# Kernel tuning notes

Measured on AMD Instinct MI355X. Metric: run time of the kernel, lower is better.

## Reference

```python
import jax, jax.numpy as jnp
import numpy as np

# ---- fixed constants from stft2hcfp.__init__ ----
FS = 16000.0; FR = 2.0; FC = 27.5; TC = 1.0 / 4487.0; NPO = 48
N = int(FS / FR)                      # 8000 FFT length
HALF_N = int(round(N / 2))            # 4000
SQRT_N = float(np.sqrt(N))
HIGH_FREQ_IDX = int(round(1.0 / TC / FR) + 1)   # 2245
HIGH_QUEF_IDX = int(round(FS / FC)) + 1         # 583
CUT_Q = int(round(FS * TC))           # 4  (cepstrum cutoff)
TOTAL_BINS = 4 * 88                   # 352 log-freq bins
NUM_HARMONIC = 5

def _central_freqs():
    stop = 1.0 / TC
    nest = int(np.ceil(np.log2(stop / FC)) * NPO)
    cf = []
    for i in range(nest):
        c = FC * 2.0 ** (float(i) / NPO)
        if c < stop:
            cf.append(c)
        else:
            break
    return cf

CF = _central_freqs()   # 353 central frequencies
NEST = len(CF)

def _freq_matrix():
    # triangular log-frequency filterbank over linear freq axis
    f = (FS * np.linspace(0, 0.5, HALF_N, endpoint=True))[:HIGH_FREQ_IDX]
    W = np.zeros((NEST - 1, len(f)), np.float32)
    for i in range(1, NEST - 1):
        l = int(round(CF[i - 1] / FR)); r = int(round(CF[i + 1] / FR) + 1)
        if l >= r - 1:
            W[i, l] = 1.0
        else:
            for j in range(l, r):
                if CF[i - 1] < f[j] < CF[i]:
                    W[i, j] = (f[j] - CF[i - 1]) / (CF[i] - CF[i - 1])
                elif CF[i] < f[j] < CF[i + 1]:
                    W[i, j] = (CF[i + 1] - f[j]) / (CF[i + 1] - CF[i])
    return W

def _quef_matrix():
    q = np.arange(HIGH_QUEF_IDX) / FS + 1e-6
    fq = 1.0 / q
    W = np.zeros((NEST - 1, len(fq)), np.float32)
    for i in range(1, NEST - 1):
        for j in range(int(round(FS / CF[i + 1])), int(round(FS / CF[i - 1]) + 1)):
            if j >= len(fq):
                continue
            if CF[i - 1] < fq[j] < CF[i]:
                W[i, j] = (fq[j] - CF[i - 1]) / (CF[i] - CF[i - 1])
            elif CF[i] < fq[j] < CF[i + 1]:
                W[i, j] = (CF[i + 1] - fq[j]) / (CF[i + 1] - CF[i])
    return W

# harmonic shift indices: closest central freq to (k+1)*27.5 Hz, k=0..5
HIDS = [int(np.argmin(np.abs(np.asarray(CF) - (k + 1) * FC))) for k in range(NUM_HARMONIC + 1)]


def _nonlinear(x, g, cutoff):
    # relu + pow(g), then zero first/last `cutoff` rows along axis 1.
    # safe pow: grad is 0 where x<=0 (matches relu-masked torch behavior, no inf at 0)
    y = jnp.where(x > 0, jnp.where(x > 0, x, 1.0) ** g, 0.0)
    y = y.at[:, :cutoff].set(0.0).at[:, -cutoff:].set(0.0)
    return y


def setup_inputs() -> dict:
    key = jax.random.key(0)
    dx = jax.random.uniform(key, (8, 512, N), dtype=jnp.float32)  # [B, T, 8000] spectrogram
    return {
        "dx": dx,
        "W_freq": jnp.asarray(_freq_matrix()),   # [352, 2245]
        "W_quef": jnp.asarray(_quef_matrix()),   # [352, 583]
    }


def reference(dx, W_freq, W_quef):
    tfr0 = jnp.swapaxes(dx, 1, 2)                       # [B, F=8000, T]
    # CFP layer 1: real part of FFT over freq axis -> cepstrum, nonlinear g=0.6
    ceps = jnp.fft.fft(tfr0, axis=1).real / SQRT_N      # [B, 8000, T]
    ceps = _nonlinear(ceps, 0.6, CUT_Q)
    # log-frequency mappings (banded triangular filterbanks)
    tfr0h = tfr0[:, :HIGH_FREQ_IDX]                      # [B, 2245, T]
    cepsh = ceps[:, :HIGH_QUEF_IDX]                      # [B, 583, T]
    tfrL0 = jnp.einsum('kf,bft->bkt', W_freq, tfr0h)     # [B, 352, T]
    tfrLQ = jnp.einsum('kq,bqt->bkt', W_quef, cepsh)     # [B, 352, T]
    # harmonic stacking: shift down (spectral) / shift up (cepstral)
    har_s = [jnp.pad(tfrL0[:, h:TOTAL_BINS], ((0, 0), (0, h), (0, 0))) for h in HIDS]
    har_c = [jnp.pad(tfrLQ[:, :TOTAL_BINS - h], ((0, 0), (h, 0), (0, 0))) for h in HIDS]
    piece = jnp.concatenate([jnp.stack(har_s, axis=1), jnp.stack(har_c, axis=1)], axis=1)
    return jnp.swapaxes(piece, 2, 3)                     # [B, 12, T, 352]
```

## Files before the change

kernel.cpp:

```cpp
#include <hip/hip_runtime.h>
#include <hip/hip_bf16.h>
#include <limits.h>

typedef __attribute__((ext_vector_type(8))) short short8;
typedef __attribute__((ext_vector_type(4))) float f32x4;
typedef __attribute__((ext_vector_type(4))) int i32x4;
typedef __attribute__((ext_vector_type(16))) float f32x16;

#define NN 8000
#define NCOL 4096
#define KBINS 352
#define QPAD 640
#define QH 320
#define BN 256
#define KC 8
#define NTILE 64
#define KSTEP 8
#define XROW 4096
#define CUTQ 4
#define T_ 512
#define WFB 64
#define WQB 20
#define NFB 4096
#define NCB 640

#define GLL16(g, l) __builtin_amdgcn_global_load_lds( \
    (const __attribute__((address_space(1))) unsigned int*)(g), \
    (__attribute__((address_space(3))) unsigned int*)(l), 16, 0, 0)

static __device__ __forceinline__ ushort bfc(float f){
  __hip_bfloat16 h = __float2bfloat16(f);
  return *reinterpret_cast<ushort*>(&h);
}
static __device__ __forceinline__ float b2f(ushort u){
  unsigned v = ((unsigned)u) << 16; float f; __builtin_memcpy(&f, &v, 4); return f;
}

__global__ __launch_bounds__(256) void prep_k(const float* __restrict__ dx,
        ushort* __restrict__ xf, ushort* __restrict__ cosg,
        const float* __restrict__ Wf, const float* __restrict__ Wq,
        int HFI, int HQI, int* __restrict__ fLo, int* __restrict__ qLo,
        float* __restrict__ WfT, float* __restrict__ WqT){
  int blk = blockIdx.x, t = threadIdx.x;
  if (blk < NFB){
    int row = blk;
    int w = t >> 6, l = t & 63;
    const float* rp = dx + (size_t)row*NN;
    ushort* xrow = xf + (size_t)row*XROW;
    f32x4 F0[2], F1[2], M0[2], M1[2];
    int n0g[2], N0g[2];
    #pragma unroll
    for (int g=0; g<2; ++g){
      int N0 = (2*w + g)*512;
      int n0 = N0 + 8*l;
      N0g[g] = N0; n0g[g] = n0;
      F0[g] = *(const f32x4*)(rp + n0);
      F1[g] = *(const f32x4*)(rp + n0 + 4);
      int mb = 8000 - N0 - 511 + 8*l;
      bool sh = (N0 == 0 && l == 63);
      M0[g] = *(const f32x4*)(rp + mb);
      M1[g] = *(const f32x4*)(rp + mb + (sh ? 3 : 4));
    }
    #pragma unroll
    for (int g=0; g<2; ++g){
      float a[8];
      #pragma unroll
      for (int i=0;i<4;i++) a[i]   = __shfl(M0[g][i], 63 - l, 64);
      #pragma unroll
      for (int i=0;i<4;i++) a[4+i] = __shfl(M1[g][i], 63 - l, 64);
      float fw[8] = {F0[g][0],F0[g][1],F0[g][2],F0[g][3],F1[g][0],F1[g][1],F1[g][2],F1[g][3]};
      bool comp = (N0g[g] == 0 && l == 0);
      short8 o;
      #pragma unroll
      for (int e=0;e<8;e++){
        int n = n0g[g] + e;
        int mi = 7 - e;
        if (comp && e >= 1 && e <= 4) mi = 8 - e;
        float v;
        if (n == 0)          v = fw[0];
        else if (n < 4000)   v = fw[e] + a[mi];
        else if (n == 4000)  v = fw[e];
        else                 v = 0.f;
        o[e] = (short)bfc(v);
      }
      *(short8*)(xrow + n0g[g]) = o;
    }
  } else if (blk < NFB + NCB){
    int q = blk - NFB;
    int qz = (q < HQI) ? 1 : 0;
    #pragma unroll
    for (int h=0; h<2; ++h){
      int n0 = t*16 + h*8;
      short8 o;
      #pragma unroll
      for (int e=0;e<8;e++){
        float v = 0.f;
        if (qz){
          int m = (q*(n0+e)) % NN;
          v = cosf((float)m * 7.8539816339744831e-4f);
        }
        o[e] = (short)bfc(v);
      }
      int kt = n0 >> 6, s8 = (n0 >> 3) & 7;
      *(short8*)(&cosg[(size_t)kt*(QPAD*64) + (size_t)q*64 + ((s8 ^ (q & 7)) << 3)]) = o;
    }
  } else {
    __shared__ int slo, shi;
    int u = blk - NFB - NCB;
    int r = u >> 1;
    bool isF = (u & 1) == 0;
    const float* W = isF ? Wf : Wq;
    int width = isF ? HFI : HQI;
    int bw    = isF ? WFB : WQB;
    float* WT = isF ? WfT : WqT;
    int* Lo   = isF ? fLo : qLo;
    if (t==0){ slo = INT_MAX; shi = -1; }
    __syncthreads();
    int mylo = INT_MAX, myhi = -1;
    for (int c = t; c < width; c += 256){
      if (W[(size_t)r*width + c] != 0.f){ if (c < mylo) mylo = c; if (c > myhi) myhi = c; }
    }
    atomicMin(&slo, mylo); atomicMax(&shi, myhi);
    __syncthreads();
    int l = (shi < 0) ? 0 : slo, h = (shi < 0) ? 0 : shi + 1;
    if (t==0) Lo[r] = l;
    for (int j = t; j < bw; j += 256){
      float v = 0.f;
      if (l + j < h) v = W[(size_t)r*width + l + j];
      WT[(size_t)j*KBINS + r] = v;
    }
  }
}

__global__ __launch_bounds__(512, 2) void gemm_k(const ushort* __restrict__ xf,
                                                 const ushort* __restrict__ cosg,
                                                 ushort* __restrict__ part){
  __shared__ ushort As[2][QH*64];
  __shared__ ushort Bs[2][BN*64];
  int tid = threadIdx.x;
  int nb = blockIdx.x, qh = blockIdx.y, kc = blockIdx.z;
  int lane = tid & 63, widx = tid >> 6;
  int wm = widx & 1, wn = widx >> 1;
  int l31 = lane & 31, lh = lane >> 5;
  int kt0 = kc*KSTEP, ktE = kt0 + KSTEP;

  const ushort* ag0 = cosg + (size_t)qh*(QH*64) + tid*8;
  int brow0 = tid >> 3, bs = tid & 7;
  const ushort* bg0 = xf + ((size_t)(nb*BN + brow0))*XROW + bs*8;
  int bw0 = brow0*64 + ((bs ^ (brow0 & 7)) << 3);

  i32x4 Breg[4];
  #define AGLL(kt_, buf_) { \
    const ushort* ag_ = ag0 + (size_t)(kt_)*(QPAD*64); \
    _Pragma("unroll") \
    for (int i_=0;i_<5;i_++) GLL16(ag_ + i_*4096, &As[buf_][tid*8 + i_*4096]); }
  #define BLOAD(kt_) { \
    _Pragma("unroll") \
    for (int i_=0;i_<4;i_++) Breg[i_] = *(const i32x4*)(bg0 + (size_t)i_*64*XROW + (kt_)*64); }
  #define BWRITE(buf_) { \
    _Pragma("unroll") \
    for (int i_=0;i_<4;i_++) *(i32x4*)(&Bs[buf_][bw0 + i_*4096]) = Breg[i_]; }

  f32x16 acc[5][2];
  #pragma unroll
  for (int a=0;a<5;a++){ acc[a][0] = (f32x16)0.f; acc[a][1] = (f32x16)0.f; }

  BLOAD(kt0);
  AGLL(kt0, 0);
  asm volatile("s_waitcnt vmcnt(5)" ::: "memory");
  BWRITE(0);
  asm volatile("s_waitcnt vmcnt(0) lgkmcnt(0)" ::: "memory");
  __builtin_amdgcn_s_barrier();
  __builtin_amdgcn_sched_barrier(0);

  int cur = 0;
  for (int kt = kt0; kt < ktE; ++kt){
    bool stg = (kt + 1 < ktE);
    if (stg){
      BLOAD(kt+1);
      AGLL(kt+1, cur^1);
    }
    __builtin_amdgcn_sched_barrier(0);
    const ushort* Ac = &As[cur][0];
    const ushort* Bc = &Bs[cur][0];
    #pragma unroll
    for (int p=0;p<4;p++){
      short8 dfr[2];
      #pragma unroll
      for (int c=0;c<2;c++){
        int row = wn*64 + c*32 + l31;
        dfr[c] = *(const short8*)(Bc + row*64 + ((((p<<1)|lh) ^ (row & 7)) << 3));
      }
      short8 cfr[5];
      #pragma unroll
      for (int a=0;a<5;a++){
        int row = wm*160 + a*32 + l31;
        cfr[a] = *(const short8*)(Ac + row*64 + ((((p<<1)|lh) ^ (row & 7)) << 3));
      }
      __builtin_amdgcn_s_setprio(1);
      #pragma unroll
      for (int a=0;a<5;a++){
        acc[a][0] = __builtin_amdgcn_mfma_f32_32x32x16_bf16(dfr[0], cfr[a], acc[a][0], 0,0,0);
        acc[a][1] = __builtin_amdgcn_mfma_f32_32x32x16_bf16(dfr[1], cfr[a], acc[a][1], 0,0,0);
      }
      __builtin_amdgcn_s_setprio(0);
      if (p < 3){
        __builtin_amdgcn_sched_barrier(0);
        __builtin_amdgcn_s_barrier();
        __builtin_amdgcn_sched_barrier(0);
      }
    }
    if (stg){
      __builtin_amdgcn_sched_barrier(0);
      asm volatile("s_waitcnt vmcnt(5)" ::: "memory");
      BWRITE(cur^1);
      asm volatile("s_waitcnt vmcnt(0) lgkmcnt(0)" ::: "memory");
      __builtin_amdgcn_s_barrier();
      __builtin_amdgcn_sched_barrier(0);
    }
    cur ^= 1;
  }

  ushort* pb = part + (size_t)kc*NCOL*QPAD;
  #pragma unroll
  for (int a=0;a<5;a++){
    int q = qh*QH + wm*160 + a*32 + l31;
    #pragma unroll
    for (int c=0;c<2;c++){
      int colb = nb*BN + wn*64 + c*32 + 4*lh;
      #pragma unroll
      for (int r=0;r<16;r++){
        int col = colb + (r&3) + 8*(r>>2);
        pb[(size_t)col*QPAD + q] = bfc(acc[a][c][r]);
      }
    }
  }
}

__global__ __launch_bounds__(384) void fuse_k(const float* __restrict__ dx,
        const ushort* __restrict__ part,
        const float* __restrict__ WfT, const float* __restrict__ WqT,
        const int* __restrict__ fLo, const int* __restrict__ qLo,
        float* __restrict__ out, int HFI, int HQI){
  __shared__ float xr[2368];
  __shared__ float yq[QPAD];
  __shared__ float tl0[KBINS];
  __shared__ float tlq[KBINS];
  int col = blockIdx.x;
  int b = col >> 9, t = col & 511;
  int tid = threadIdx.x;
  const float invs = 0.011180339887498949f;

  for (int f = tid; f < 2368; f += 384) xr[f] = (f < HFI) ? dx[(size_t)col*NN + f] : 0.f;
  const ushort* pc = part + (size_t)col*QPAD;
  for (int q = tid; q < QPAD; q += 384){
    float y = 0.f;
    if (q < HQI){
      float s = 0.f;
      #pragma unroll
      for (int kc=0; kc<KC; kc++) s += b2f(pc[(size_t)kc*NCOL*QPAD + q]);
      s *= invs;
      if (q >= CUTQ && s > 0.f) y = powf(s, 0.6f);
    }
    yq[q] = y;
  }
  __syncthreads();

  if (tid < KBINS){
    int k = tid;
    int lo = fLo[k];
    float aF = 0.f;
    #pragma unroll
    for (int j=0;j<WFB;j++) aF += WfT[j*KBINS + k] * xr[lo + j];
    int ql = qLo[k];
    float aQ = 0.f;
    #pragma unroll
    for (int j=0;j<WQB;j++) aQ += WqT[j*KBINS + k] * yq[ql + j];
    tl0[k] = aF; tlq[k] = aQ;
  }
  __syncthreads();

  const int hids[6] = {0,48,76,96,111,124};
  for (int u = tid; u < 12*KBINS; u += 384){
    int j = u / KBINS;
    int k = u - j*KBINS;
    int h = hids[(j < 6) ? j : j - 6];
    float v;
    if (j < 6) v = (k + h < KBINS) ? tl0[k + h] : 0.f;
    else       v = (k >= h)        ? tlq[k - h] : 0.f;
    out[(((size_t)b*12 + j)*T_ + t)*KBINS + k] = v;
  }
}

extern "C" void kernel_launch(void* const* d_in, const int* in_sizes, int n_in,
                              void* d_out, int out_size, void* d_ws, size_t ws_size,
                              hipStream_t stream){
  const float* dx = (const float*)d_in[0];
  const float* Wf = (const float*)d_in[1];
  const float* Wq = (const float*)d_in[2];
  int HFI = in_sizes[1] / KBINS;
  int HQI = in_sizes[2] / KBINS;
  float* out = (float*)d_out;
  char* ws = (char*)d_ws;

  ushort* cosg = (ushort*)ws;
  size_t off = (size_t)NTILE*QPAD*64*2;
  ushort* xf = (ushort*)(ws + off); off += (size_t)NCOL*XROW*2;
  ushort* part = (ushort*)(ws + off); off += (size_t)KC*NCOL*QPAD*2;
  int* fLo = (int*)(ws+off); off += KBINS*4;
  int* qLo = (int*)(ws+off); off += KBINS*4;
  float* WfT = (float*)(ws+off); off += (size_t)WFB*KBINS*4;
  float* WqT = (float*)(ws+off); off += (size_t)WQB*KBINS*4;
  (void)n_in; (void)out_size; (void)ws_size;

  prep_k<<<NFB + NCB + 2*KBINS, 256, 0, stream>>>(dx, xf, cosg, Wf, Wq,
                                                  HFI, HQI, fLo, qLo, WfT, WqT);
  gemm_k<<<dim3(NCOL/BN, QPAD/QH, KC), 512, 0, stream>>>(xf, cosg, part);
  fuse_k<<<NCOL, 384, 0, stream>>>(dx, part, WfT, WqT, fLo, qLo, out, HFI, HQI);
}
```

Before: 125.2 us.

## Split cosine GEMM by quefrency parity using half-period even/odd input folding

Replaces the mirror fold x[n]+x[N-n] with a half-period fold: since cos(2πq(n+N/2)/N) = (-1)^q·cos(2πqn/N), even quefrencies use x[n]+x[n+4000] and odd ones use x[n]-x[n+4000]. prep_k now writes two folded inputs from contiguous loads, with no wave shuffles, and writes a parity-split cosine table. The GEMM y-dimension now selects parity instead of a quefrency half, and fuse_k remaps q to the parity slot. This simplifies the prep stage, but each GEMM block now streams its own parity-specific input matrix rather than sharing one, which doubles input traffic and workspace.

```diff
diff --git a/kernel.cpp b/kernel.cpp
--- a/kernel.cpp
+++ b/kernel.cpp
@@ -17,6 +17,7 @@
 #define NTILE 64
 #define KSTEP 8
 #define XROW 4096
+#define XPAR ((size_t)NCOL*XROW)
 #define CUTQ 4
 #define T_ 512
 #define WFB 64
@@ -37,56 +38,52 @@
 }
 
 __global__ __launch_bounds__(256) void prep_k(const float* __restrict__ dx,
-        ushort* __restrict__ xf, ushort* __restrict__ cosg,
+        ushort* __restrict__ xs, ushort* __restrict__ cosp,
         const float* __restrict__ Wf, const float* __restrict__ Wq,
         int HFI, int HQI, int* __restrict__ fLo, int* __restrict__ qLo,
         float* __restrict__ WfT, float* __restrict__ WqT){
   int blk = blockIdx.x, t = threadIdx.x;
   if (blk < NFB){
     int row = blk;
-    int w = t >> 6, l = t & 63;
     const float* rp = dx + (size_t)row*NN;
-    ushort* xrow = xf + (size_t)row*XROW;
-    f32x4 F0[2], F1[2], M0[2], M1[2];
-    int n0g[2], N0g[2];
+    ushort* xe = xs + (size_t)row*XROW;
+    ushort* xo = xs + XPAR + (size_t)row*XROW;
+    f32x4 A[2][2], B[2][2];
+    int n0g[2]; bool live[2];
     #pragma unroll
     for (int g=0; g<2; ++g){
-      int N0 = (2*w + g)*512;
-      int n0 = N0 + 8*l;
-      N0g[g] = N0; n0g[g] = n0;
-      F0[g] = *(const f32x4*)(rp + n0);
-      F1[g] = *(const f32x4*)(rp + n0 + 4);
-      int mb = 8000 - N0 - 511 + 8*l;
-      bool sh = (N0 == 0 && l == 63);
-      M0[g] = *(const f32x4*)(rp + mb);
-      M1[g] = *(const f32x4*)(rp + mb + (sh ? 3 : 4));
+      int n0 = g*2048 + t*8;
+      n0g[g] = n0; live[g] = (n0 < 4000);
+      if (live[g]){
+        A[g][0] = *(const f32x4*)(rp + n0);
+        A[g][1] = *(const f32x4*)(rp + n0 + 4);
+        B[g][0] = *(const f32x4*)(rp + 4000 + n0);
+        B[g][1] = *(const f32x4*)(rp + 4000 + n0 + 4);
+      }
     }
     #pragma unroll
     for (int g=0; g<2; ++g){
-      float a[8];
-      #pragma unroll
-      for (int i=0;i<4;i++) a[i]   = __shfl(M0[g][i], 63 - l, 64);
-      #pragma unroll
-      for (int i=0;i<4;i++) a[4+i] = __shfl(M1[g][i], 63 - l, 64);
-      float fw[8] = {F0[g][0],F0[g][1],F0[g][2],F0[g][3],F1[g][0],F1[g][1],F1[g][2],F1[g][3]};
-      bool comp = (N0g[g] == 0 && l == 0);
-      short8 o;
-      #pragma unroll
-      for (int e=0;e<8;e++){
-        int n = n0g[g] + e;
-        int mi = 7 - e;
-        if (comp && e >= 1 && e <= 4) mi = 8 - e;
-        float v;
-        if (n == 0)          v = fw[0];
-        else if (n < 4000)   v = fw[e] + a[mi];
-        else if (n == 4000)  v = fw[e];
-        else                 v = 0.f;
-        o[e] = (short)bfc(v);
-      }
-      *(short8*)(xrow + n0g[g]) = o;
+      short8 oe, oo;
+      if (live[g]){
+        #pragma unroll
+        for (int i=0;i<2;i++){
+          #pragma unroll
+          for (int e=0;e<4;e++){
+            float a = A[g][i][e], b = B[g][i][e];
+            oe[4*i+e] = (short)bfc(a + b);
+            oo[4*i+e] = (short)bfc(a - b);
+          }
+        }
+      } else {
+        #pragma unroll
+        for (int e=0;e<8;e++){ oe[e] = 0; oo[e] = 0; }
+      }
+      *(short8*)(xe + n0g[g]) = oe;
+      *(short8*)(xo + n0g[g]) = oo;
     }
   } else if (blk < NFB + NCB){
     int q = blk - NFB;
+    int par = q & 1, u = q >> 1;
     int qz = (q < HQI) ? 1 : 0;
     #pragma unroll
     for (int h=0; h<2; ++h){
@@ -95,14 +92,16 @@
       #pragma unroll
       for (int e=0;e<8;e++){
         float v = 0.f;
-        if (qz){
-          int m = (q*(n0+e)) % NN;
+        int n = n0 + e;
+        if (qz && n < 4000){
+          int m = (q*n) % NN;
           v = cosf((float)m * 7.8539816339744831e-4f);
         }
         o[e] = (short)bfc(v);
       }
       int kt = n0 >> 6, s8 = (n0 >> 3) & 7;
-      *(short8*)(&cosg[(size_t)kt*(QPAD*64) + (size_t)q*64 + ((s8 ^ (q & 7)) << 3)]) = o;
+      *(short8*)(&cosp[((size_t)par*NTILE + kt)*(QH*64) + (size_t)u*64
+                       + ((s8 ^ (u & 7)) << 3)]) = o;
     }
   } else {
     __shared__ int slo, shi;
@@ -132,26 +131,26 @@
   }
 }
 
-__global__ __launch_bounds__(512, 2) void gemm_k(const ushort* __restrict__ xf,
-                                                 const ushort* __restrict__ cosg,
+__global__ __launch_bounds__(512, 2) void gemm_k(const ushort* __restrict__ xs,
+                                                 const ushort* __restrict__ cosp,
                                                  ushort* __restrict__ part){
   __shared__ ushort As[2][QH*64];
   __shared__ ushort Bs[2][BN*64];
   int tid = threadIdx.x;
-  int nb = blockIdx.x, qh = blockIdx.y, kc = blockIdx.z;
+  int nb = blockIdx.x, par = blockIdx.y, kc = blockIdx.z;
   int lane = tid & 63, widx = tid >> 6;
   int wm = widx & 1, wn = widx >> 1;
   int l31 = lane & 31, lh = lane >> 5;
   int kt0 = kc*KSTEP, ktE = kt0 + KSTEP;
 
-  const ushort* ag0 = cosg + (size_t)qh*(QH*64) + tid*8;
+  const ushort* ag0 = cosp + (size_t)par*(NTILE*QH*64) + tid*8;
   int brow0 = tid >> 3, bs = tid & 7;
-  const ushort* bg0 = xf + ((size_t)(nb*BN + brow0))*XROW + bs*8;
+  const ushort* bg0 = xs + (size_t)par*XPAR + (size_t)(nb*BN + brow0)*XROW + bs*8;
   int bw0 = brow0*64 + ((bs ^ (brow0 & 7)) << 3);
 
   i32x4 Breg[4];
   #define AGLL(kt_, buf_) { \
-    const ushort* ag_ = ag0 + (size_t)(kt_)*(QPAD*64); \
+    const ushort* ag_ = ag0 + (size_t)(kt_)*(QH*64); \
     _Pragma("unroll") \
     for (int i_=0;i_<5;i_++) GLL16(ag_ + i_*4096, &As[buf_][tid*8 + i_*4096]); }
   #define BLOAD(kt_) { \
@@ -224,14 +223,14 @@
   ushort* pb = part + (size_t)kc*NCOL*QPAD;
   #pragma unroll
   for (int a=0;a<5;a++){
-    int q = qh*QH + wm*160 + a*32 + l31;
+    int slot = par*QH + wm*160 + a*32 + l31;
     #pragma unroll
     for (int c=0;c<2;c++){
       int colb = nb*BN + wn*64 + c*32 + 4*lh;
       #pragma unroll
       for (int r=0;r<16;r++){
         int col = colb + (r&3) + 8*(r>>2);
-        pb[(size_t)col*QPAD + q] = bfc(acc[a][c][r]);
+        pb[(size_t)col*QPAD + slot] = bfc(acc[a][c][r]);
       }
     }
   }
@@ -256,9 +255,10 @@
   for (int q = tid; q < QPAD; q += 384){
     float y = 0.f;
     if (q < HQI){
+      int slot = (q & 1)*QH + (q >> 1);
       float s = 0.f;
       #pragma unroll
-      for (int kc=0; kc<KC; kc++) s += b2f(pc[(size_t)kc*NCOL*QPAD + q]);
+      for (int kc=0; kc<KC; kc++) s += b2f(pc[(size_t)kc*NCOL*QPAD + slot]);
       s *= invs;
       if (q >= CUTQ && s > 0.f) y = powf(s, 0.6f);
     }
@@ -303,9 +303,9 @@
   float* out = (float*)d_out;
   char* ws = (char*)d_ws;
 
-  ushort* cosg = (ushort*)ws;
-  size_t off = (size_t)NTILE*QPAD*64*2;
-  ushort* xf = (ushort*)(ws + off); off += (size_t)NCOL*XROW*2;
+  ushort* cosp = (ushort*)ws;
+  size_t off = (size_t)2*NTILE*QH*64*2;
+  ushort* xs = (ushort*)(ws + off); off += (size_t)2*NCOL*XROW*2;
   ushort* part = (ushort*)(ws + off); off += (size_t)KC*NCOL*QPAD*2;
   int* fLo = (int*)(ws+off); off += KBINS*4;
   int* qLo = (int*)(ws+off); off += KBINS*4;
@@ -313,8 +313,8 @@
   float* WqT = (float*)(ws+off); off += (size_t)WQB*KBINS*4;
   (void)n_in; (void)out_size; (void)ws_size;
 
-  prep_k<<<NFB + NCB + 2*KBINS, 256, 0, stream>>>(dx, xf, cosg, Wf, Wq,
+  prep_k<<<NFB + NCB + 2*KBINS, 256, 0, stream>>>(dx, xs, cosp, Wf, Wq,
                                                   HFI, HQI, fLo, qLo, WfT, WqT);
-  gemm_k<<<dim3(NCOL/BN, QPAD/QH, KC), 512, 0, stream>>>(xf, cosg, part);
+  gemm_k<<<dim3(NCOL/BN, 2, KC), 512, 0, stream>>>(xs, cosp, part);
   fuse_k<<<NCOL, 384, 0, stream>>>(dx, part, WfT, WqT, fLo, qLo, out, HFI, HQI);
 }
```

After: 132.2 us. 5.6% more time.
